# Kernel optimization log

Measured on AMD Instinct MI355X. Metric: run time of the kernel, lower is better.

The kernel has to match this reference:

```python
import jax, jax.numpy as jnp
import numpy as np

FEAT_DIM = 2048
H_DIM = 1024
N = 8192  # num_obj (tree nodes in pre-order traversal order)


def setup_inputs() -> dict:
    key = jax.random.key(0)
    ks = jax.random.split(key, 5)
    features = jax.random.normal(ks[0], (N, FEAT_DIM), dtype=jnp.float32)
    # block_orthogonal init approximated by scaled gaussian (same math at runtime)
    Wx = jax.random.normal(ks[1], (4 * H_DIM, FEAT_DIM), dtype=jnp.float32) / np.sqrt(FEAT_DIM)
    Wh = jax.random.normal(ks[2], (4 * H_DIM, H_DIM), dtype=jnp.float32) / np.sqrt(H_DIM)
    bx = jnp.zeros((4 * H_DIM,), dtype=jnp.float32)
    # iofuh bias: forget-gate block [2h:3h] filled with 1.0
    bh = jnp.zeros((4 * H_DIM,), dtype=jnp.float32).at[2 * H_DIM:3 * H_DIM].set(1.0)
    # binary tree in pre-order-compatible (topological) order: parent of t is (t-1)//2 < t; root = -1
    t = jnp.arange(N)
    parent_idx = jnp.where(t == 0, -1, (t - 1) // 2).astype(jnp.int32)
    root_c = jax.random.normal(ks[3], (1, H_DIM), dtype=jnp.float32)
    root_h = jax.random.normal(ks[4], (1, H_DIM), dtype=jnp.float32)
    return {"features": features, "Wx": Wx, "bx": bx, "Wh": Wh, "bh": bh,
            "parent_idx": parent_idx, "root_c": root_c, "root_h": root_h}


def reference(features, Wx, bx, Wh, bh, parent_idx, root_c, root_h):
    # Precompute the input projection for ALL nodes with one big GEMM
    # (the original does this per-node; math is identical).
    xproj = features @ Wx.T + (bx + bh)  # [N, 4H]
    WhT = Wh.T  # [H, 4H]
    # state buffers; slot 0 holds the root state, slot t+1 holds node t's state
    h_buf = jnp.concatenate([root_h, jnp.zeros((N, H_DIM), features.dtype)], axis=0)  # [N+1, H]
    c_buf = jnp.concatenate([root_c, jnp.zeros((N, H_DIM), features.dtype)], axis=0)

    def step(carry, inp):
        h_buf, c_buf = carry
        t, p, xp = inp
        hp = h_buf[p + 1]  # parent hidden [H]
        cp = c_buf[p + 1]  # parent cell   [H]
        iofu = xp + hp @ WhT  # [4H]
        i, o, f, u = jnp.split(iofu, 4)
        i = jax.nn.sigmoid(i)
        o = jax.nn.sigmoid(o)
        f = jax.nn.sigmoid(f)
        u = jnp.tanh(u)
        c = i * u + f * cp
        h = o * jnp.tanh(c)
        h_buf = h_buf.at[t + 1].set(h)
        c_buf = c_buf.at[t + 1].set(c)
        return (h_buf, c_buf), h

    ts = jnp.arange(N)
    (_, _), hidden = jax.lax.scan(step, (h_buf, c_buf), (ts, parent_idx, xproj))
    return hidden  # [N, H] == treelstm_io.hidden rows in traversal order
```

## Files before the change

### kernel.cpp

```cpp
#include <hip/hip_runtime.h>
#include <hip/hip_fp16.h>
#include <math.h>

#define FEAT 2048
#define HD 1024
#define FH 4096
#define NN 8192

using s16x8 = __attribute__((ext_vector_type(8))) short;
using f32x4 = __attribute__((ext_vector_type(4))) float;

#define GLOBAL_AS __attribute__((address_space(1)))
#define LDS_AS __attribute__((address_space(3)))

__device__ __forceinline__ void gload_lds16(const void* g, void* l) {
    __builtin_amdgcn_global_load_lds((const GLOBAL_AS unsigned int*)g,
                                     (LDS_AS unsigned int*)l, 16, 0, 0);
}

__device__ __forceinline__ unsigned short f2bf(float f) {
    union { float f; unsigned u; } v; v.f = f;
    unsigned r = v.u + 0x7FFFu + ((v.u >> 16) & 1u);
    return (unsigned short)(r >> 16);
}

__device__ __forceinline__ float fast_sig(float x) { return 1.0f / (1.0f + __expf(-x)); }
__device__ __forceinline__ float fast_tanh(float x) {
    float ax = fabsf(x);
    float e = __expf(2.0f * ax);
    float r = 1.0f - 2.0f / (e + 1.0f);
    return copysignf(r, x);
}

__global__ __launch_bounds__(256) void convert_all_kernel(
    const float* __restrict__ feat, const float* __restrict__ Wx,
    const float* __restrict__ Wh, unsigned short* __restrict__ feat_b,
    unsigned short* __restrict__ Wx_b, unsigned short* __restrict__ Wh_b,
    const float* __restrict__ root_h, const float* __restrict__ root_c,
    unsigned short* __restrict__ h_buf, float* __restrict__ c_buf,
    int* __restrict__ done)
{
    const size_t g = (size_t)blockIdx.x * 256 + threadIdx.x;
    if (g < HD) { h_buf[g] = f2bf(root_h[g]); c_buf[g] = root_c[g]; }
    if (g < 16) done[g] = 0;

    const size_t n1 = (size_t)NN * FEAT;
    const size_t n2 = n1 + (size_t)FH * FEAT;
    size_t i = g * 8;
    const float* s; unsigned short* d;
    if (i < n1)      { s = feat + i;        d = feat_b + i; }
    else if (i < n2) { s = Wx + (i - n1);   d = Wx_b + (i - n1); }
    else             { s = Wh + (i - n2);   d = Wh_b + (i - n2); }
    float4 a = *(const float4*)s;
    float4 b = *(const float4*)(s + 4);
    unsigned short r[8] = {f2bf(a.x), f2bf(a.y), f2bf(a.z), f2bf(a.w),
                           f2bf(b.x), f2bf(b.y), f2bf(b.z), f2bf(b.w)};
    *(s16x8*)d = *(const s16x8*)r;
}

__global__ __launch_bounds__(512, 2) void xproj_8ph(
    const unsigned short* __restrict__ Ab,
    const unsigned short* __restrict__ Bb,
    const float* __restrict__ bx, const float* __restrict__ bh,
    __half* __restrict__ xproj)
{
    __shared__ char lds[131072];
    const int tid = threadIdx.x;
    const int wid = tid >> 6;
    const int lane = tid & 63;
    const int wr = wid >> 2;
    const int wc = wid & 3;
    const int bm = blockIdx.x * 256;
    const int bn = blockIdx.y * 256;
    const int fr = lane & 15;
    const int fq = lane >> 4;

    const int srow = tid >> 3;
    const int sslot = (tid & 7) ^ (srow & 7);
    const unsigned short* gA[4];
    const unsigned short* gB[4];
    #pragma unroll
    for (int q = 0; q < 4; ++q) {
        gA[q] = Ab + (size_t)(bm + q * 64 + srow) * FEAT + sslot * 8;
        gB[q] = Bb + (size_t)(bn + q * 64 + srow) * FEAT + sslot * 8;
    }
    const int ldsoff = tid * 16;

    f32x4 acc[8][4];
    #pragma unroll
    for (int i = 0; i < 8; ++i)
        #pragma unroll
        for (int j = 0; j < 4; ++j) { f32x4 z = {0.f, 0.f, 0.f, 0.f}; acc[i][j] = z; }

    #pragma unroll
    for (int q = 0; q < 4; ++q) {
        gload_lds16(gA[q], lds + q * 8192 + ldsoff);
        gload_lds16(gB[q], lds + 32768 + q * 8192 + ldsoff);
    }

    for (int t = 0; t < 32; ++t) {
        const int d = t & 1;
        const char* LA = lds + d * 65536;
        const char* LB = LA + 32768;
        char* SA = lds + (d ^ 1) * 65536;
        char* SB = SA + 32768;
        const int knext = (t + 1) * 64;

        asm volatile("s_waitcnt vmcnt(0)" ::: "memory");
        __builtin_amdgcn_s_barrier();

        #pragma unroll
        for (int kk = 0; kk < 2; ++kk) {
            const int kbyte = kk * 64 + fq * 16;
            s16x8 aF[8], bF[4];
            #pragma unroll
            for (int i = 0; i < 8; ++i) {
                const int row = wr * 128 + i * 16 + fr;
                aF[i] = *(const s16x8*)(LA + row * 128 + (kbyte ^ ((row & 7) << 4)));
            }
            #pragma unroll
            for (int j = 0; j < 4; ++j) {
                const int row = wc * 64 + j * 16 + fr;
                bF[j] = *(const s16x8*)(LB + row * 128 + (kbyte ^ ((row & 7) << 4)));
            }
            if (t < 31) {
                if (kk == 0) {
                    #pragma unroll
                    for (int q = 0; q < 4; ++q)
                        gload_lds16(gA[q] + knext, SA + q * 8192 + ldsoff);
                } else {
                    #pragma unroll
                    for (int q = 0; q < 4; ++q)
                        gload_lds16(gB[q] + knext, SB + q * 8192 + ldsoff);
                }
            }
            __builtin_amdgcn_s_setprio(1);
            #pragma unroll
            for (int i = 0; i < 8; ++i)
                #pragma unroll
                for (int j = 0; j < 4; ++j)
                    acc[i][j] = __builtin_amdgcn_mfma_f32_16x16x32_bf16(
                        aF[i], bF[j], acc[i][j], 0, 0, 0);
            __builtin_amdgcn_s_setprio(0);
        }
    }

    __builtin_amdgcn_s_barrier();
    char* W = lds + wid * 16384;
    #pragma unroll
    for (int j = 0; j < 4; ++j) {
        const int c_loc = j * 16 + fr;
        const int col = bn + wc * 64 + c_loc;
        const float bias = bx[col] + bh[col];
        #pragma unroll
        for (int i = 0; i < 8; ++i) {
            #pragma unroll
            for (int reg = 0; reg < 4; ++reg) {
                const int r_loc = i * 16 + fq * 4 + reg;
                const int byteo = r_loc * 128 +
                    ((((c_loc >> 3) ^ (r_loc & 7)) << 4)) + (c_loc & 7) * 2;
                *(__half*)(W + byteo) = __float2half_rn(acc[i][j][reg] + bias);
            }
        }
    }
    asm volatile("s_waitcnt lgkmcnt(0)" ::: "memory");
    #pragma unroll
    for (int k = 0; k < 16; ++k) {
        const int f = k * 64 + lane;
        const int r_loc = f >> 3;
        const int cchunk = f & 7;
        const s16x8 v = *(const s16x8*)(W + r_loc * 128 +
                                        ((cchunk ^ (r_loc & 7)) << 4));
        const int grow = bm + wr * 128 + r_loc;
        const int gcol = bn + wc * 64 + cchunk * 8;
        *(s16x8*)((unsigned short*)xproj + (size_t)grow * FH + gcol) = v;
    }
}

__global__ __launch_bounds__(512, 2) void levels_fused_small(
    const __half* __restrict__ xproj, const unsigned short* __restrict__ Whb,
    unsigned short* __restrict__ h_buf, float* __restrict__ c_buf,
    float* __restrict__ out, int* __restrict__ done)
{
    constexpr int MR = 4;
    constexpr int ABYTES = 128 * 128;
    constexpr int BUF = ABYTES + 32768;
    __shared__ char lds[2 * BUF];
    const int bid = blockIdx.x;
    int lvl, nb;
    if (bid < 128)      { lvl = bid >> 4; nb = 0; }
    else if (bid < 160) { lvl = 8;        nb = (bid - 128) >> 4; }
    else                { lvl = 9;        nb = (bid - 160) >> 4; }
    const int jg0 = (bid & 15) * 64;
    const int start = (1 << lvl) - 1;
    const int cnt = 1 << lvl;
    const int lim = start + cnt;
    const int t0 = start + nb * 128;

    if (lvl > 0) {
        if (threadIdx.x == 0) {
            const int need = (lvl <= 8) ? 16 : 32;
            while (__hip_atomic_load(done + (lvl - 1), __ATOMIC_RELAXED,
                                     __HIP_MEMORY_SCOPE_AGENT) < need)
                __builtin_amdgcn_s_sleep(16);
        }
        __syncthreads();
        __builtin_amdgcn_fence(__ATOMIC_ACQUIRE, "agent");
    }

    const int tid = threadIdx.x;
    const int wid = tid >> 6, lane = tid & 63;
    const int wr = wid >> 2, wc = wid & 3;
    const int fr = lane & 15, fq = lane >> 4;

    const int srow = tid >> 3;
    const int sslot = (tid & 7) ^ (srow & 7);
    const unsigned short* gA[2];
    #pragma unroll
    for (int q = 0; q < 2; ++q) {
        const int rg = min(nb * 128 + q * 64 + srow, cnt - 1);
        const int arow = ((start + rg - 1) >> 1) + 1;
        gA[q] = h_buf + (size_t)arow * HD + sslot * 8;
    }
    const unsigned short* gB[4];
    #pragma unroll
    for (int q = 0; q < 4; ++q) {
        const int r = q * 64 + srow;
        const int whrow = ((r >> 4) & 3) * 1024 + jg0 + ((r >> 6) * 16) + (r & 15);
        gB[q] = Whb + (size_t)whrow * HD + sslot * 8;
    }
    const int ldsoff = tid * 16;

    f32x4 acc[MR][4];
    #pragma unroll
    for (int i = 0; i < MR; ++i)
        #pragma unroll
        for (int j = 0; j < 4; ++j) { f32x4 z = {0.f, 0.f, 0.f, 0.f}; acc[i][j] = z; }

    #pragma unroll
    for (int q = 0; q < 2; ++q)
        gload_lds16(gA[q], lds + q * 8192 + ldsoff);
    #pragma unroll
    for (int q = 0; q < 4; ++q)
        gload_lds16(gB[q], lds + ABYTES + q * 8192 + ldsoff);

    for (int t = 0; t < 16; ++t) {
        const char* LA = lds + (t & 1) * BUF;
        const char* LB = LA + ABYTES;
        char* SA = lds + ((t & 1) ^ 1) * BUF;
        char* SB = SA + ABYTES;
        const int knext = (t + 1) * 64;

        asm volatile("s_waitcnt vmcnt(0)" ::: "memory");
        __builtin_amdgcn_s_barrier();

        #pragma unroll
        for (int kk = 0; kk < 2; ++kk) {
            const int kbyte = kk * 64 + fq * 16;
            s16x8 aF[MR], bF[4];
            #pragma unroll
            for (int i = 0; i < MR; ++i) {
                const int row = wr * 64 + i * 16 + fr;
                aF[i] = *(const s16x8*)(LA + row * 128 + (kbyte ^ ((row & 7) << 4)));
            }
            #pragma unroll
            for (int j = 0; j < 4; ++j) {
                const int row = wc * 64 + j * 16 + fr;
                bF[j] = *(const s16x8*)(LB + row * 128 + (kbyte ^ ((row & 7) << 4)));
            }
            if (t < 15) {
                if (kk == 0) {
                    #pragma unroll
                    for (int q = 0; q < 2; ++q)
                        gload_lds16(gA[q] + knext, SA + q * 8192 + ldsoff);
                } else {
                    #pragma unroll
                    for (int q = 0; q < 4; ++q)
                        gload_lds16(gB[q] + knext, SB + q * 8192 + ldsoff);
                }
            }
            __builtin_amdgcn_s_setprio(1);
            #pragma unroll
            for (int i = 0; i < MR; ++i)
                #pragma unroll
                for (int j = 0; j < 4; ++j)
                    acc[i][j] = __builtin_amdgcn_mfma_f32_16x16x32_bf16(
                        aF[i], bF[j], acc[i][j], 0, 0, 0);
            __builtin_amdgcn_s_setprio(0);
        }
    }

    const int col = jg0 + wc * 16 + fr;
    #pragma unroll
    for (int i = 0; i < MR; ++i) {
        #pragma unroll
        for (int reg = 0; reg < 4; ++reg) {
            const int t = t0 + wr * 64 + i * 16 + fq * 4 + reg;
            if (t < lim) {
                const int prow = ((t - 1) >> 1) + 1;
                const size_t xb = (size_t)t * FH + col;
                const float gi = acc[i][0][reg] + __half2float(xproj[xb]);
                const float go = acc[i][1][reg] + __half2float(xproj[xb + HD]);
                const float gf = acc[i][2][reg] + __half2float(xproj[xb + 2 * HD]);
                const float gu = acc[i][3][reg] + __half2float(xproj[xb + 3 * HD]);
                const float cp = c_buf[(size_t)prow * HD + col];
                const float c = fast_sig(gi) * fast_tanh(gu) + fast_sig(gf) * cp;
                const float h = fast_sig(go) * fast_tanh(c);
                c_buf[(size_t)(t + 1) * HD + col] = c;
                h_buf[(size_t)(t + 1) * HD + col] = f2bf(h);
                out[(size_t)t * HD + col] = h;
            }
        }
    }

    __syncthreads();
    if (threadIdx.x == 0)
        __hip_atomic_fetch_add(done + lvl, 1, __ATOMIC_RELEASE,
                               __HIP_MEMORY_SCOPE_AGENT);
}

template<int BM>
__global__ __launch_bounds__(512, 2) void level_kk(
    const __half* __restrict__ xproj, const unsigned short* __restrict__ Whb,
    int start, int prevstart, unsigned short* __restrict__ h_buf,
    float* __restrict__ c_buf, float* __restrict__ out)
{
    constexpr int MR = BM / 32;
    constexpr int ABYTES = BM * 128;
    constexpr int BUF = ABYTES + 32768;
    __shared__ char lds[2 * BUF];
    const int tid = threadIdx.x;
    const int wid = tid >> 6, lane = tid & 63;
    const int wr = wid >> 2, wc = wid & 3;
    const int fr = lane & 15, fq = lane >> 4;
    const int t0 = start + blockIdx.x * BM;
    const int jg0 = blockIdx.y * 64;

    const int srow = tid >> 3;
    const int sslot = (tid & 7) ^ (srow & 7);
    const unsigned short* gA[BM / 64];
    #pragma unroll
    for (int q = 0; q < BM / 64; ++q) {
        const int rg = blockIdx.x * BM + q * 64 + srow;
        gA[q] = h_buf + (size_t)(prevstart + (rg >> 1) + 1) * HD + sslot * 8;
    }
    const unsigned short* gB[4];
    #pragma unroll
    for (int q = 0; q < 4; ++q) {
        const int r = q * 64 + srow;
        const int whrow = ((r >> 4) & 3) * 1024 + jg0 + ((r >> 6) * 16) + (r & 15);
        gB[q] = Whb + (size_t)whrow * HD + sslot * 8;
    }
    const int ldsoff = tid * 16;

    f32x4 acc[MR][4];
    #pragma unroll
    for (int i = 0; i < MR; ++i)
        #pragma unroll
        for (int j = 0; j < 4; ++j) { f32x4 z = {0.f, 0.f, 0.f, 0.f}; acc[i][j] = z; }

    #pragma unroll
    for (int q = 0; q < BM / 64; ++q)
        gload_lds16(gA[q], lds + q * 8192 + ldsoff);
    #pragma unroll
    for (int q = 0; q < 4; ++q)
        gload_lds16(gB[q], lds + ABYTES + q * 8192 + ldsoff);

    for (int t = 0; t < 16; ++t) {
        const char* LA = lds + (t & 1) * BUF;
        const char* LB = LA + ABYTES;
        char* SA = lds + ((t & 1) ^ 1) * BUF;
        char* SB = SA + ABYTES;
        const int knext = (t + 1) * 64;

        asm volatile("s_waitcnt vmcnt(0)" ::: "memory");
        __builtin_amdgcn_s_barrier();

        #pragma unroll
        for (int kk = 0; kk < 2; ++kk) {
            const int kbyte = kk * 64 + fq * 16;
            s16x8 aF[MR], bF[4];
            #pragma unroll
            for (int i = 0; i < MR; ++i) {
                const int row = wr * (BM / 2) + i * 16 + fr;
                aF[i] = *(const s16x8*)(LA + row * 128 + (kbyte ^ ((row & 7) << 4)));
            }
            #pragma unroll
            for (int j = 0; j < 4; ++j) {
                const int row = wc * 64 + j * 16 + fr;
                bF[j] = *(const s16x8*)(LB + row * 128 + (kbyte ^ ((row & 7) << 4)));
            }
            if (t < 15) {
                if (kk == 0) {
                    #pragma unroll
                    for (int q = 0; q < BM / 64; ++q)
                        gload_lds16(gA[q] + knext, SA + q * 8192 + ldsoff);
                } else {
                    #pragma unroll
                    for (int q = 0; q < 4; ++q)
                        gload_lds16(gB[q] + knext, SB + q * 8192 + ldsoff);
                }
            }
            __builtin_amdgcn_s_setprio(1);
            #pragma unroll
            for (int i = 0; i < MR; ++i)
                #pragma unroll
                for (int j = 0; j < 4; ++j)
                    acc[i][j] = __builtin_amdgcn_mfma_f32_16x16x32_bf16(
                        aF[i], bF[j], acc[i][j], 0, 0, 0);
            __builtin_amdgcn_s_setprio(0);
        }
    }

    const int col = jg0 + wc * 16 + fr;
    #pragma unroll
    for (int i = 0; i < MR; ++i) {
        #pragma unroll
        for (int reg = 0; reg < 4; ++reg) {
            const int t = t0 + wr * (BM / 2) + i * 16 + fq * 4 + reg;
            const int p = (t - 1) >> 1;
            const size_t xb = (size_t)t * FH + col;
            const float gi = acc[i][0][reg] + __half2float(xproj[xb]);
            const float go = acc[i][1][reg] + __half2float(xproj[xb + HD]);
            const float gf = acc[i][2][reg] + __half2float(xproj[xb + 2 * HD]);
            const float gu = acc[i][3][reg] + __half2float(xproj[xb + 3 * HD]);
            const float cp = c_buf[(size_t)(p + 1) * HD + col];
            const float c = fast_sig(gi) * fast_tanh(gu) + fast_sig(gf) * cp;
            const float h = fast_sig(go) * fast_tanh(c);
            c_buf[(size_t)(t + 1) * HD + col] = c;
            h_buf[(size_t)(t + 1) * HD + col] = f2bf(h);
            out[(size_t)t * HD + col] = h;
        }
    }
}

__device__ __forceinline__ void bk128_issue(
    const unsigned short* const (&gA)[8], const unsigned short* const (&gB)[8],
    int k0, unsigned short* As, unsigned short* Bs, int wbase)
{
    #pragma unroll
    for (int q = 0; q < 8; ++q) {
        gload_lds16(gA[q] + k0, (char*)As + q * 4096 + wbase);
        gload_lds16(gB[q] + k0, (char*)Bs + q * 4096 + wbase);
    }
}

__device__ __forceinline__ void bk128_compute(
    const unsigned short* As, const unsigned short* Bs,
    f32x4 (&acc)[4][4], int wm, int wn16, int fr, int fkb)
{
    #pragma unroll
    for (int kk = 0; kk < 4; ++kk) {
        s16x8 aF[4], bF[4];
        #pragma unroll
        for (int i = 0; i < 4; ++i) {
            const int r = wm + i * 16 + fr;
            const int byteIn = (kk * 64 + fkb) ^ ((r & 7) << 4);
            aF[i] = *(const s16x8*)((const char*)As + r * 256 + byteIn);
        }
        #pragma unroll
        for (int g = 0; g < 4; ++g) {
            const int r = g * 32 + wn16 + fr;
            const int byteIn = (kk * 64 + fkb) ^ ((r & 7) << 4);
            bF[g] = *(const s16x8*)((const char*)Bs + r * 256 + byteIn);
        }
        #pragma unroll
        for (int i = 0; i < 4; ++i)
            #pragma unroll
            for (int g = 0; g < 4; ++g)
                acc[i][g] = __builtin_amdgcn_mfma_f32_16x16x32_bf16(aF[i], bF[g], acc[i][g], 0, 0, 0);
    }
}

__global__ __launch_bounds__(256) void level_bk128_dbuf(
    const __half* __restrict__ xproj, const unsigned short* __restrict__ Whb,
    const int* __restrict__ parent, unsigned short* __restrict__ h_buf,
    float* __restrict__ c_buf, float* __restrict__ out,
    int start, int count)
{
    __shared__ unsigned short As0[128 * 128];
    __shared__ unsigned short Bs0[128 * 128];
    __shared__ unsigned short As1[128 * 128];
    __shared__ unsigned short Bs1[128 * 128];
    const int tid = threadIdx.x;
    const int wid = tid >> 6;
    const int lane = tid & 63;
    const int t0 = start + blockIdx.x * 128;
    const int jg0 = blockIdx.y * 32;
    const int lim = start + count;
    const int wm = (wid & 1) * 64;
    const int wn16 = (wid >> 1) * 16;
    const int wbase = wid * 1024;
    const int srow_b = tid >> 4;
    const int rowbyte = (tid & 15) * 16;

    const unsigned short* gA[8];
    const unsigned short* gB[8];
    #pragma unroll
    for (int q = 0; q < 8; ++q) {
        const int r = q * 16 + srow_b;
        const int sk = (rowbyte ^ ((r & 7) << 4)) >> 1;
        const int tA = min(t0 + r, lim - 1);
        gA[q] = h_buf + (size_t)(parent[tA] + 1) * HD + sk;
        const int whrow = ((r >> 5) << 10) + jg0 + (r & 31);
        gB[q] = Whb + (size_t)whrow * HD + sk;
    }

    f32x4 acc[4][4];
    #pragma unroll
    for (int i = 0; i < 4; ++i)
        #pragma unroll
        for (int g = 0; g < 4; ++g) { f32x4 z = {0.f, 0.f, 0.f, 0.f}; acc[i][g] = z; }

    const int fr = lane & 15;
    const int fkb = (lane >> 4) * 16;

    bk128_issue(gA, gB, 0, As0, Bs0, wbase);
    #pragma unroll
    for (int t = 0; t < 8; ++t) {
        unsigned short* curA = (t & 1) ? As1 : As0;
        unsigned short* curB = (t & 1) ? Bs1 : Bs0;
        unsigned short* nxtA = (t & 1) ? As0 : As1;
        unsigned short* nxtB = (t & 1) ? Bs0 : Bs1;
        if (t < 7) {
            bk128_issue(gA, gB, (t + 1) * 128, nxtA, nxtB, wbase);
            asm volatile("s_waitcnt vmcnt(16)" ::: "memory");
        } else {
            asm volatile("s_waitcnt vmcnt(0)" ::: "memory");
        }
        __builtin_amdgcn_s_barrier();
        __builtin_amdgcn_sched_barrier(0);
        bk128_compute(curA, curB, acc, wm, wn16, fr, fkb);
        __builtin_amdgcn_sched_barrier(0);
        __builtin_amdgcn_s_barrier();
    }

    const int col = jg0 + wn16 + fr;
    const int fq = lane >> 4;
    #pragma unroll
    for (int i = 0; i < 4; ++i) {
        #pragma unroll
        for (int reg = 0; reg < 4; ++reg) {
            const int t = t0 + wm + i * 16 + fq * 4 + reg;
            if (t < lim) {
                const int p = parent[t];
                const size_t xb = (size_t)t * FH + col;
                const float gi = acc[i][0][reg] + __half2float(xproj[xb]);
                const float go = acc[i][1][reg] + __half2float(xproj[xb + HD]);
                const float gf = acc[i][2][reg] + __half2float(xproj[xb + 2 * HD]);
                const float gu = acc[i][3][reg] + __half2float(xproj[xb + 3 * HD]);
                const float cp = c_buf[(size_t)(p + 1) * HD + col];
                const float c = fast_sig(gi) * fast_tanh(gu) + fast_sig(gf) * cp;
                const float h = fast_sig(go) * fast_tanh(c);
                c_buf[(size_t)(t + 1) * HD + col] = c;
                h_buf[(size_t)(t + 1) * HD + col] = f2bf(h);
                out[(size_t)t * HD + col] = h;
            }
        }
    }
}

extern "C" void kernel_launch(void* const* d_in, const int* in_sizes, int n_in,
                              void* d_out, int out_size, void* d_ws, size_t ws_size,
                              hipStream_t stream) {
    const float* feat   = (const float*)d_in[0];
    const float* Wx     = (const float*)d_in[1];
    const float* bx     = (const float*)d_in[2];
    const float* Wh     = (const float*)d_in[3];
    const float* bh     = (const float*)d_in[4];
    const int*   parent = (const int*)d_in[5];
    const float* root_c = (const float*)d_in[6];
    const float* root_h = (const float*)d_in[7];
    float* out = (float*)d_out;

    char* ws = (char*)d_ws;
    __half* xproj = (__half*)ws;                        ws += (size_t)NN * FH * 2;
    float* c_buf = (float*)ws;                          ws += (size_t)(NN + 1) * HD * 4;
    unsigned short* feat_b = (unsigned short*)ws;       ws += (size_t)NN * FEAT * 2;
    unsigned short* Wx_b = (unsigned short*)ws;         ws += (size_t)FH * FEAT * 2;
    unsigned short* Wh_b = (unsigned short*)ws;         ws += (size_t)FH * HD * 2;
    unsigned short* h_buf = (unsigned short*)ws;        ws += (size_t)(NN + 1) * HD * 2;
    int* done = (int*)ws;                               ws += 256;

    const size_t ntot = (size_t)NN * FEAT + (size_t)FH * FEAT + (size_t)FH * HD;
    convert_all_kernel<<<(unsigned)(ntot / 8 / 256), 256, 0, stream>>>(
        feat, Wx, Wh, feat_b, Wx_b, Wh_b, root_h, root_c, h_buf, c_buf, done);

    dim3 g1(NN / 256, FH / 256);
    xproj_8ph<<<g1, 512, 0, stream>>>(feat_b, Wx_b, bx, bh, xproj);

    levels_fused_small<<<224, 512, 0, stream>>>(
        xproj, Wh_b, h_buf, c_buf, out, done);

    dim3 gl(16, 16);
    level_kk<64><<<gl, 512, 0, stream>>>(xproj, Wh_b, 1023, 511,
                                         h_buf, c_buf, out);
    level_kk<128><<<gl, 512, 0, stream>>>(xproj, Wh_b, 2047, 1023,
                                          h_buf, c_buf, out);
    level_kk<256><<<gl, 512, 0, stream>>>(xproj, Wh_b, 4095, 2047,
                                          h_buf, c_buf, out);

    dim3 g3(1, HD / 32);
    level_bk128_dbuf<<<g3, 256, 0, stream>>>(
        xproj, Wh_b, parent, h_buf, c_buf, out, 8191, 1);
}
```

Before: 453.2 us.

## Replace acquire/release fences with agent-scope atomic loads/stores in fused small-level kernel

The small-levels persistent kernel drops the agent-scope acquire fence and release atomic. Instead, inter-block h/c state is read and written with relaxed agent-scope atomic loads and stores, which bypass the non-coherent caches. The A-operand (parent hidden) is now staged through registers with explicit LDS stores rather than direct global-to-LDS loads, the K loop is fully unrolled, and the spin sleep is shortened. The aim is to cut cache-flush and invalidate cost at each level handoff. It risks memory-ordering bugs, since correctness now relies on relaxed atomics plus a vmcnt wait, and adds an extra barrier per K step.

```diff
diff --git a/kernel.cpp b/kernel.cpp
--- a/kernel.cpp
+++ b/kernel.cpp
@@ -9,6 +9,7 @@
 
 using s16x8 = __attribute__((ext_vector_type(8))) short;
 using f32x4 = __attribute__((ext_vector_type(4))) float;
+using u32x4 = __attribute__((ext_vector_type(4))) unsigned int;
 
 #define GLOBAL_AS __attribute__((address_space(1)))
 #define LDS_AS __attribute__((address_space(3)))
@@ -30,6 +31,16 @@
     float e = __expf(2.0f * ax);
     float r = 1.0f - 2.0f / (e + 1.0f);
     return copysignf(r, x);
+}
+
+__device__ __forceinline__ unsigned mall_load_u32(const unsigned* p) {
+    return __hip_atomic_load(p, __ATOMIC_RELAXED, __HIP_MEMORY_SCOPE_AGENT);
+}
+__device__ __forceinline__ void mall_store_u32(unsigned* p, unsigned v) {
+    __hip_atomic_store(p, v, __ATOMIC_RELAXED, __HIP_MEMORY_SCOPE_AGENT);
+}
+__device__ __forceinline__ void mall_store_u16(unsigned short* p, unsigned short v) {
+    __hip_atomic_store(p, v, __ATOMIC_RELAXED, __HIP_MEMORY_SCOPE_AGENT);
 }
 
 __global__ __launch_bounds__(256) void convert_all_kernel(
@@ -184,8 +195,9 @@
 {
     constexpr int MR = 4;
     constexpr int ABYTES = 128 * 128;
-    constexpr int BUF = ABYTES + 32768;
-    __shared__ char lds[2 * BUF];
+    constexpr int BBYTES = 32768;
+    __shared__ char ldsA[2 * ABYTES];
+    __shared__ char ldsB[2 * BBYTES];
     const int bid = blockIdx.x;
     int lvl, nb;
     if (bid < 128)      { lvl = bid >> 4; nb = 0; }
@@ -202,10 +214,10 @@
             const int need = (lvl <= 8) ? 16 : 32;
             while (__hip_atomic_load(done + (lvl - 1), __ATOMIC_RELAXED,
                                      __HIP_MEMORY_SCOPE_AGENT) < need)
-                __builtin_amdgcn_s_sleep(16);
+                __builtin_amdgcn_s_sleep(4);
         }
         __syncthreads();
-        __builtin_amdgcn_fence(__ATOMIC_ACQUIRE, "agent");
+        asm volatile("" ::: "memory");
     }
 
     const int tid = threadIdx.x;
@@ -215,12 +227,12 @@
 
     const int srow = tid >> 3;
     const int sslot = (tid & 7) ^ (srow & 7);
-    const unsigned short* gA[2];
+    const unsigned* gA[2];
     #pragma unroll
     for (int q = 0; q < 2; ++q) {
         const int rg = min(nb * 128 + q * 64 + srow, cnt - 1);
         const int arow = ((start + rg - 1) >> 1) + 1;
-        gA[q] = h_buf + (size_t)arow * HD + sslot * 8;
+        gA[q] = (const unsigned*)(h_buf + (size_t)arow * HD + sslot * 8);
     }
     const unsigned short* gB[4];
     #pragma unroll
@@ -237,21 +249,42 @@
         #pragma unroll
         for (int j = 0; j < 4; ++j) { f32x4 z = {0.f, 0.f, 0.f, 0.f}; acc[i][j] = z; }
 
+    unsigned aR[2][2][4];
     #pragma unroll
     for (int q = 0; q < 2; ++q)
-        gload_lds16(gA[q], lds + q * 8192 + ldsoff);
+        #pragma unroll
+        for (int w = 0; w < 4; ++w)
+            aR[0][q][w] = mall_load_u32(gA[q] + w);
     #pragma unroll
     for (int q = 0; q < 4; ++q)
-        gload_lds16(gB[q], lds + ABYTES + q * 8192 + ldsoff);
-
+        gload_lds16(gB[q], ldsB + q * 8192 + ldsoff);
+
+    #pragma unroll
     for (int t = 0; t < 16; ++t) {
-        const char* LA = lds + (t & 1) * BUF;
-        const char* LB = LA + ABYTES;
-        char* SA = lds + ((t & 1) ^ 1) * BUF;
-        char* SB = SA + ABYTES;
-        const int knext = (t + 1) * 64;
+        const char* LA = ldsA + (t & 1) * ABYTES;
+        const char* LB = ldsB + (t & 1) * BBYTES;
 
         asm volatile("s_waitcnt vmcnt(0)" ::: "memory");
+        __builtin_amdgcn_s_barrier();
+
+        #pragma unroll
+        for (int q = 0; q < 2; ++q)
+            *(u32x4*)(ldsA + (t & 1) * ABYTES + q * 8192 + ldsoff) =
+                *(const u32x4*)aR[t & 1][q];
+
+        if (t < 15) {
+            #pragma unroll
+            for (int q = 0; q < 2; ++q)
+                #pragma unroll
+                for (int w = 0; w < 4; ++w)
+                    aR[(t + 1) & 1][q][w] = mall_load_u32(gA[q] + (t + 1) * 32 + w);
+            #pragma unroll
+            for (int q = 0; q < 4; ++q)
+                gload_lds16(gB[q] + (t + 1) * 64,
+                            ldsB + ((t + 1) & 1) * BBYTES + q * 8192 + ldsoff);
+        }
+
+        asm volatile("s_waitcnt lgkmcnt(0)" ::: "memory");
         __builtin_amdgcn_s_barrier();
 
         #pragma unroll
@@ -267,17 +300,6 @@
             for (int j = 0; j < 4; ++j) {
                 const int row = wc * 64 + j * 16 + fr;
                 bF[j] = *(const s16x8*)(LB + row * 128 + (kbyte ^ ((row & 7) << 4)));
-            }
-            if (t < 15) {
-                if (kk == 0) {
-                    #pragma unroll
-                    for (int q = 0; q < 2; ++q)
-                        gload_lds16(gA[q] + knext, SA + q * 8192 + ldsoff);
-                } else {
-                    #pragma unroll
-                    for (int q = 0; q < 4; ++q)
-                        gload_lds16(gB[q] + knext, SB + q * 8192 + ldsoff);
-                }
             }
             __builtin_amdgcn_s_setprio(1);
             #pragma unroll
@@ -299,23 +321,26 @@
             if (t < lim) {
                 const int prow = ((t - 1) >> 1) + 1;
                 const size_t xb = (size_t)t * FH + col;
+                union { unsigned u; float f; } cpv;
+                cpv.u = mall_load_u32((const unsigned*)(c_buf + (size_t)prow * HD + col));
                 const float gi = acc[i][0][reg] + __half2float(xproj[xb]);
                 const float go = acc[i][1][reg] + __half2float(xproj[xb + HD]);
                 const float gf = acc[i][2][reg] + __half2float(xproj[xb + 2 * HD]);
                 const float gu = acc[i][3][reg] + __half2float(xproj[xb + 3 * HD]);
-                const float cp = c_buf[(size_t)prow * HD + col];
-                const float c = fast_sig(gi) * fast_tanh(gu) + fast_sig(gf) * cp;
+                const float c = fast_sig(gi) * fast_tanh(gu) + fast_sig(gf) * cpv.f;
                 const float h = fast_sig(go) * fast_tanh(c);
-                c_buf[(size_t)(t + 1) * HD + col] = c;
-                h_buf[(size_t)(t + 1) * HD + col] = f2bf(h);
+                union { float f; unsigned u; } cv; cv.f = c;
+                mall_store_u32((unsigned*)(c_buf + (size_t)(t + 1) * HD + col), cv.u);
+                mall_store_u16(h_buf + (size_t)(t + 1) * HD + col, f2bf(h));
                 out[(size_t)t * HD + col] = h;
             }
         }
     }
 
+    asm volatile("s_waitcnt vmcnt(0)" ::: "memory");
     __syncthreads();
     if (threadIdx.x == 0)
-        __hip_atomic_fetch_add(done + lvl, 1, __ATOMIC_RELEASE,
+        __hip_atomic_fetch_add(done + lvl, 1, __ATOMIC_RELAXED,
                                __HIP_MEMORY_SCOPE_AGENT);
 }
 
```

After: 547.1 us. 20.7% more time.
